# Performance work log

Measured on AMD Instinct MI355X. Metric: run time of the kernel, lower is better.

## Reference

```python
import jax, jax.numpy as jnp
import numpy as np

EPS = 1e-5

def gather_neighbour(pc, idx):
    # pc: [B,N,d], idx: [B,Q,k] -> [B,Q,k,d]
    return jax.vmap(lambda p, i: p[i])(pc, idx)

def rel_pos_encoding(q_xyz, src_xyz, idx):
    # q_xyz: [B,Q,3], src_xyz: [B,N,3], idx: [B,Q,k] -> [B,Q,k,10]
    nbr = gather_neighbour(src_xyz, idx)              # [B,Q,k,3]
    tile = q_xyz[:, :, None, :]                       # [B,Q,1,3]
    rel = tile - nbr                                  # [B,Q,k,3]
    dis = jnp.sqrt(jnp.sum(rel * rel, axis=-1, keepdims=True))
    tile_b = jnp.broadcast_to(tile, nbr.shape)
    return jnp.concatenate([dis, rel, tile_b, nbr], axis=-1)

def conv_bn_relu(x, W, g, b, m, v):
    # 1x1 conv (bias-free) + inference BatchNorm + ReLU; x: [B,Q,K,Cin], W: [Cout,Cin]
    y = jnp.einsum('bqkc,oc->bqko', x, W)
    y = (y - m) * (g * jax.lax.rsqrt(v + EPS)) + b
    return jax.nn.relu(y)

def att_pool(x, Wfc, Wm, g, b, m, v):
    # x: [B,Q,K,C] -> [B,Q,1,Cout]; softmax over neighbor axis K
    att = jnp.einsum('bqkc,oc->bqko', x, Wfc)
    att = jax.nn.softmax(att, axis=2)
    agg = jnp.sum(x * att, axis=2, keepdims=True)     # [B,Q,1,C]
    return conv_bn_relu(agg, Wm, g, b, m, v)

def setup_inputs() -> dict:
    key = jax.random.key(0)
    ks = jax.random.split(key, 40)
    B, Q, k, Nd, Ns = 2, 16384, 16, 4096, 16384
    dim_lb, dim_sc, dim_nl = 128, 64, 128
    d_mid = dim_lb + 10 - dim_sc   # 74
    d_att = dim_lb + 10            # 138
    f32 = jnp.float32
    inp = {}
    inp['features_lb'] = jax.random.normal(ks[0], (B, Q, k, dim_lb), f32)
    inp['features_sc'] = jax.random.normal(ks[1], (B, Q, k, dim_sc), f32)
    inp['NM_lb'] = jax.random.randint(ks[2], (B, Q, k), 0, Nd)
    inp['NM_sc'] = jax.random.randint(ks[3], (B, Q, k), 0, Ns)
    inp['coords_lb'] = jax.random.normal(ks[4], (B, Nd, 3), f32)
    inp['coords_sc'] = jax.random.normal(ks[5], (B, Ns, 3), f32)
    inp['coords_queries'] = jax.random.normal(ks[6], (B, Q, 3), f32)
    inp['NM_cl'] = jax.random.randint(ks[7], (B, Q, k), 0, Q)
    def bn(i, c):
        return (jax.random.uniform(ks[i], (c,), f32) + 0.5,
                jax.random.normal(ks[i + 1], (c,), f32) * 0.1,
                jax.random.normal(ks[i + 2], (c,), f32) * 0.1,
                jax.random.uniform(ks[i + 3], (c,), f32) + 0.5)
    inp['W_lb'] = jax.random.normal(ks[8], (10, 10), f32) * 0.3
    inp['g_lb'], inp['b_lb'], inp['m_lb'], inp['v_lb'] = bn(9, 10)
    inp['W_sc'] = jax.random.normal(ks[13], (d_mid, 10), f32) * 0.3
    inp['g_sc'], inp['b_sc'], inp['m_sc'], inp['v_sc'] = bn(14, d_mid)
    inp['W_fc1'] = jax.random.normal(ks[18], (d_att, d_att), f32) * 0.08
    inp['W_mlp1'] = jax.random.normal(ks[19], (dim_nl, d_att), f32) * 0.08
    inp['g1'], inp['b1'], inp['m1'], inp['v1'] = bn(20, dim_nl)
    inp['W_cl'] = jax.random.normal(ks[24], (10, 10), f32) * 0.3
    inp['g_cl'], inp['b_cl'], inp['m_cl'], inp['v_cl'] = bn(25, 10)
    inp['W_fc2'] = jax.random.normal(ks[29], (d_att, d_att), f32) * 0.08
    inp['W_mlp2'] = jax.random.normal(ks[30], (dim_nl, d_att), f32) * 0.08
    inp['g2'], inp['b2'], inp['m2'], inp['v2'] = bn(31, dim_nl)
    return inp

def reference(features_lb, features_sc, NM_lb, NM_sc, coords_lb, coords_sc,
              coords_queries, NM_cl,
              W_lb, g_lb, b_lb, m_lb, v_lb,
              W_sc, g_sc, b_sc, m_sc, v_sc,
              W_fc1, W_mlp1, g1, b1, m1, v1,
              W_cl, g_cl, b_cl, m_cl, v_cl,
              W_fc2, W_mlp2, g2, b2, m2, v2):
    # branch 1: layer-below
    rppe_lb = conv_bn_relu(rel_pos_encoding(coords_queries, coords_lb, NM_lb),
                           W_lb, g_lb, b_lb, m_lb, v_lb)          # [B,Q,k,10]
    # branch 2: skip connection
    rppe_sc = conv_bn_relu(rel_pos_encoding(coords_queries, coords_sc, NM_sc),
                           W_sc, g_sc, b_sc, m_sc, v_sc)          # [B,Q,k,74]
    locSE_lb = jnp.concatenate([rppe_lb, features_lb], axis=-1)   # [B,Q,k,138]
    locSE_sc = jnp.concatenate([rppe_sc, features_sc], axis=-1)   # [B,Q,k,138]
    f_hat = jnp.concatenate([locSE_lb, locSE_sc], axis=2)         # [B,Q,2k,138]
    f_tilde = att_pool(f_hat, W_fc1, W_mlp1, g1, b1, m1, v1)      # [B,Q,1,128]
    # second aggregation over current layer (num_agg > 1)
    rppe_cl = conv_bn_relu(rel_pos_encoding(coords_queries, coords_queries, NM_cl),
                           W_cl, g_cl, b_cl, m_cl, v_cl)          # [B,Q,k,10]
    f_cur = gather_neighbour(f_tilde[:, :, 0, :], NM_cl)          # [B,Q,k,128]
    locSE_cl = jnp.concatenate([rppe_cl, f_cur], axis=-1)         # [B,Q,k,138]
    f_tilde = att_pool(locSE_cl, W_fc2, W_mlp2, g2, b2, m2, v2)   # [B,Q,1,128]
    # match torch output layout [B, dim_nl, Q, 1]
    return jnp.transpose(f_tilde, (0, 3, 1, 2))
```

## Files before the change

### kernel.cpp

```cpp
#include <hip/hip_runtime.h>
#include <cmath>

#define EPSF 1e-5f
typedef unsigned int  uint32;
typedef unsigned short u16;
typedef __attribute__((ext_vector_type(8))) short bfrag;
typedef __attribute__((ext_vector_type(4))) float f32x4;

constexpr int Qn   = 16384;
constexpr int KS   = 168;
constexpr int PXS  = 42;
constexpr int AGS  = 168;
constexpr int Nd   = 4096;
constexpr float LOG2E = 1.4426950408889634f;

constexpr int OFF_W1  = 0;
constexpr int OFF_WM1 = 23040;
constexpr int OFF_W2  = 43520;
constexpr int OFF_WM2 = 66560;
constexpr int OFF_WLB = 87040;
constexpr int OFF_WSC = 87552;
constexpr int OFF_WCL = 90112;
constexpr int END_W   = 90624;
constexpr int BN_LB = 0;
constexpr int BN_SC = 20;
constexpr int BN_CL = 168;
constexpr int BN_M1 = 188;
constexpr int BN_M2 = 444;
constexpr int BN_TOT = 700;
constexpr int OFF_FT  = END_W + 2 * BN_TOT;
constexpr int PREP_N  = END_W + BN_TOT;

__device__ __forceinline__ u16 f2b(float f) {
    uint32 u = __float_as_uint(f);
    uint32 r = (u + 0x7fffu + ((u >> 16) & 1u)) >> 16;
    return (u16)r;
}
__device__ __forceinline__ float b2f(u16 h) {
    return __uint_as_float(((uint32)h) << 16);
}
__device__ __forceinline__ uint32 cvtpk(float a, float b) {
    uint32 r;
    asm("v_cvt_pk_bf16_f32 %0, %1, %2" : "=v"(r) : "v"(a), "v"(b));
    return r;
}
__device__ __forceinline__ u16 cvt1(float a) { return (u16)cvtpk(a, a); }
__device__ __forceinline__ float exp2_hw(float x) { return __builtin_amdgcn_exp2f(x); }

__global__ __launch_bounds__(256) void prep_weights(
    const float* __restrict__ Wfc1, const float* __restrict__ Wmlp1,
    const float* __restrict__ Wfc2, const float* __restrict__ Wmlp2,
    const float* __restrict__ Wlb,  const float* __restrict__ Wsc,
    const float* __restrict__ Wcl,
    const float* __restrict__ g_lb, const float* __restrict__ b_lb,
    const float* __restrict__ m_lb, const float* __restrict__ v_lb,
    const float* __restrict__ g_sc, const float* __restrict__ b_sc,
    const float* __restrict__ m_sc, const float* __restrict__ v_sc,
    const float* __restrict__ g_cl, const float* __restrict__ b_cl,
    const float* __restrict__ m_cl, const float* __restrict__ v_cl,
    const float* __restrict__ g1, const float* __restrict__ b1,
    const float* __restrict__ m1, const float* __restrict__ v1,
    const float* __restrict__ g2, const float* __restrict__ b2,
    const float* __restrict__ m2, const float* __restrict__ v2,
    u16* __restrict__ ws16)
{
    int i = blockIdx.x * 256 + threadIdx.x;
    if (i >= PREP_N) return;
    if (i >= END_W) {
        int j = i - END_W;
        const float *g, *bb, *m, *v; int o2;
        if (j < BN_SC)      { g = g_lb; bb = b_lb; m = m_lb; v = v_lb; o2 = j - BN_LB; }
        else if (j < BN_CL) { g = g_sc; bb = b_sc; m = m_sc; v = v_sc; o2 = j - BN_SC; }
        else if (j < BN_M1) { g = g_cl; bb = b_cl; m = m_cl; v = v_cl; o2 = j - BN_CL; }
        else if (j < BN_M2) { g = g1;   bb = b1;   m = m1;   v = v1;   o2 = j - BN_M1; }
        else                { g = g2;   bb = b2;   m = m2;   v = v2;   o2 = j - BN_M2; }
        int o = o2 >> 1;
        float sc_ = g[o] * rsqrtf(v[o] + EPSF);
        ((float*)(ws16 + END_W))[j] = (o2 & 1) ? (bb[o] - m[o] * sc_) : sc_;
        return;
    }
    int lane = (i >> 3) & 63, jj = i & 7;
    int row16 = lane & 15;
    int kf = ((lane >> 4) << 3) + jj;
    float v = 0.f;
    if (i < OFF_WLB) {
        const float* src; int nrows; int idx; bool fc = false;
        if (i < OFF_WM1)      { src = Wfc1;  nrows = 138; idx = i - OFF_W1;  fc = true; }
        else if (i < OFF_W2)  { src = Wmlp1; nrows = 128; idx = i - OFF_WM1; }
        else if (i < OFF_WM2) { src = Wfc2;  nrows = 138; idx = i - OFF_W2;  fc = true; }
        else                  { src = Wmlp2; nrows = 128; idx = i - OFF_WM2; }
        int t = idx >> 9, nt = t / 5, kt = t - nt * 5;
        int row = nt * 16 + row16;
        int kp  = kt * 32 + kf;
        int k   = (kp < 10) ? kp : kp - 2;
        if (row < nrows && kp < 140 && kp != 10 && kp != 11) {
            v = src[row * 138 + k];
            if (fc) v *= LOG2E;
        }
    } else {
        const float* src; int nrows; int idx;
        if (i < OFF_WSC)      { src = Wlb; nrows = 10; idx = i - OFF_WLB; }
        else if (i < OFF_WCL) { src = Wsc; nrows = 74; idx = i - OFF_WSC; }
        else                  { src = Wcl; nrows = 10; idx = i - OFF_WCL; }
        int t = idx >> 9;
        int row = t * 16 + row16;
        if (row < nrows && kf < 10) v = src[row * 10 + kf];
    }
    ws16[i] = f2b(v);
}

__device__ __forceinline__ void loadB(bfrag (&bf)[5], const u16* __restrict__ Wt,
                                      int nt, int lane) {
    #pragma unroll
    for (int kt = 0; kt < 5; ++kt)
        bf[kt] = *(const bfrag*)&Wt[((nt * 5 + kt) << 9) + (lane << 3)];
}
__device__ __forceinline__ void mfma32(const bfrag (&af)[2][5], const bfrag (&bf)[5],
                                       f32x4 &a0, f32x4 &a1) {
    const f32x4 zf = {0.f, 0.f, 0.f, 0.f};
    a0 = zf; a1 = zf;
    #pragma unroll
    for (int kt = 0; kt < 5; ++kt) {
        a0 = __builtin_amdgcn_mfma_f32_16x16x32_bf16(af[0][kt], bf[kt], a0, 0, 0, 0);
        a1 = __builtin_amdgcn_mfma_f32_16x16x32_bf16(af[1][kt], bf[kt], a1, 0, 0, 0);
    }
}
__device__ __forceinline__ void mfma16(const bfrag (&af)[5], const bfrag (&bf)[5],
                                       f32x4 &a0) {
    const f32x4 zf = {0.f, 0.f, 0.f, 0.f};
    a0 = zf;
    #pragma unroll
    for (int kt = 0; kt < 5; ++kt)
        a0 = __builtin_amdgcn_mfma_f32_16x16x32_bf16(af[kt], bf[kt], a0, 0, 0, 0);
}
__device__ __forceinline__ void soft32(
    const f32x4& a0, const f32x4& a1, int nt,
    int lane, int lrow, const u16* __restrict__ fr0, const u16* __restrict__ fr1,
    u16* __restrict__ ag)
{
    const int ch  = nt * 16 + lrow;
    const int chp = ch + (ch >= 10 ? 2 : 0);
    float s = 0.f, num = 0.f;
    #pragma unroll
    for (int r = 0; r < 4; ++r) {
        float e = exp2_hw(a0[r]);
        s += e;
        num += e * b2f(fr0[r * KS + chp]);
    }
    #pragma unroll
    for (int r = 0; r < 4; ++r) {
        float e = exp2_hw(a1[r]);
        s += e;
        num += e * b2f(fr1[r * KS + chp]);
    }
    s   += __shfl_xor(s, 16);   s   += __shfl_xor(s, 32);
    num += __shfl_xor(num, 16); num += __shfl_xor(num, 32);
    if (lane < 16)
        ag[chp] = cvt1((ch < 138) ? num * __builtin_amdgcn_rcpf(s) : 0.f);
}
__device__ __forceinline__ void soft16(
    const f32x4& a0, int nt,
    int lane, int lrow, const u16* __restrict__ fr0, u16* __restrict__ ag)
{
    const int ch  = nt * 16 + lrow;
    const int chp = ch + (ch >= 10 ? 2 : 0);
    float s = 0.f, num = 0.f;
    #pragma unroll
    for (int r = 0; r < 4; ++r) {
        float e = exp2_hw(a0[r]);
        s += e;
        num += e * b2f(fr0[r * KS + chp]);
    }
    s   += __shfl_xor(s, 16);   s   += __shfl_xor(s, 32);
    num += __shfl_xor(num, 16); num += __shfl_xor(num, 32);
    if (lane < 16)
        ag[chp] = cvt1((ch < 138) ? num * __builtin_amdgcn_rcpf(s) : 0.f);
}
#define SB() __builtin_amdgcn_sched_barrier(0)

__global__ __launch_bounds__(256, 4) void stage1(
    const float* __restrict__ feat_lb, const float* __restrict__ feat_sc,
    const int* __restrict__ nm_lb, const int* __restrict__ nm_sc,
    const float* __restrict__ c_lb, const float* __restrict__ c_sc,
    const float* __restrict__ c_q,
    u16* __restrict__ ws16)
{
    __shared__ __align__(16) u16 fhat[64 * KS];
    __shared__ __align__(16) u16 pxs[64 * PXS];
    u16* aggs = pxs;

    const int tid  = threadIdx.x;
    const int bq0  = blockIdx.x * 2;
    const int b    = bq0 >> 14;
    const int lane = tid & 63;
    const int w    = tid >> 6;
    const int lrow = lane & 15;
    const int lgr  = lane >> 4;
    const int q    = w >> 1;
    const int h    = w & 1;

    const u16* W1t  = ws16 + OFF_W1;
    const u16* Wm1t = ws16 + OFF_WM1;
    const float* bn = (const float*)(ws16 + END_W);
    u16* ft = ws16 + OFF_FT;

    bfrag wcv[3];
    float2 bnv[3];
    if (h == 0) {
        wcv[0] = *(const bfrag*)&ws16[OFF_WLB + (lane << 3)];
        wcv[1] = *(const bfrag*)&ws16[OFF_WSC + (lane << 3)];
        wcv[2] = *(const bfrag*)&ws16[OFF_WSC + 512 + (lane << 3)];
        bnv[0] = (lrow < 10) ? *(const float2*)&bn[BN_LB + lrow * 2] : float2{0.f, 0.f};
        bnv[1] = *(const float2*)&bn[BN_SC + lrow * 2];
        bnv[2] = *(const float2*)&bn[BN_SC + (16 + lrow) * 2];
    } else {
        #pragma unroll
        for (int t = 0; t < 3; ++t) {
            wcv[t] = *(const bfrag*)&ws16[OFF_WSC + ((2 + t) << 9) + (lane << 3)];
            int o = (2 + t) * 16 + lrow;
            bnv[t] = (o < 74) ? *(const float2*)&bn[BN_SC + o * 2] : float2{0.f, 0.f};
        }
    }

    {
        const float4* flb = (const float4*)(feat_lb + (size_t)bq0 * 2048);
        float4 r0[4];
        #pragma unroll
        for (int it = 0; it < 4; ++it) r0[it] = flb[tid + it * 256];
        const float4* fsc = (const float4*)(feat_sc + (size_t)bq0 * 1024);
        float4 r1[2];
        #pragma unroll
        for (int it = 0; it < 2; ++it) r1[it] = fsc[tid + it * 256];
        #pragma unroll
        for (int it = 0; it < 4; ++it) {
            int u = tid + it * 256;
            int qq = u >> 9, rem = u & 511, r = rem >> 5, c4 = rem & 31;
            uint32* d = (uint32*)&fhat[(qq * 32 + r) * KS + 12 + c4 * 4];
            d[0] = cvtpk(r0[it].x, r0[it].y); d[1] = cvtpk(r0[it].z, r0[it].w);
        }
        #pragma unroll
        for (int it = 0; it < 2; ++it) {
            int u = tid + it * 256;
            int qq = u >> 8, rem = u & 255, r = rem >> 4, c4 = rem & 15;
            uint32* d = (uint32*)&fhat[(qq * 32 + 16 + r) * KS + 76 + c4 * 4];
            d[0] = cvtpk(r1[it].x, r1[it].y); d[1] = cvtpk(r1[it].z, r1[it].w);
        }
        for (int u = tid; u < 64 * 15; u += 256) {
            int row = u / 15, jj = u - row * 15;
            uint32* base = (uint32*)((char*)fhat + row * 336);
            if (jj == 0) base[5] = 0u; else base[69 + jj] = 0u;
        }
    }
    if (tid < 64) {
        const int qq = tid >> 5, r = tid & 31;
        const int bq = bq0 + qq;
        const bool lb = r < 16;
        const int idx = lb ? nm_lb[bq * 16 + r] : nm_sc[bq * 16 + (r - 16)];
        const float* nb = lb ? (c_lb + ((size_t)b * Nd + idx) * 3)
                             : (c_sc + ((size_t)b * Qn + idx) * 3);
        const float qx = c_q[bq * 3 + 0], qy = c_q[bq * 3 + 1], qz = c_q[bq * 3 + 2];
        const float nx = nb[0], ny = nb[1], nz = nb[2];
        const float rx = qx - nx, ry = qy - ny, rz = qz - nz;
        const float dd = sqrtf(rx * rx + ry * ry + rz * rz);
        uint32* pw = (uint32*)&pxs[tid * PXS];
        pw[0] = cvtpk(dd, rx); pw[1] = cvtpk(ry, rz); pw[2] = cvtpk(qx, qy);
        pw[3] = cvtpk(qz, nx); pw[4] = cvtpk(ny, nz);
        #pragma unroll
        for (int z = 5; z < 16; ++z) pw[z] = 0u;
    }
    __syncthreads();

    const f32x4 zf = {0.f, 0.f, 0.f, 0.f};

    {
        bfrag pa1 = *(const bfrag*)&pxs[(q * 32 + 16 + lrow) * PXS + lgr * 8];
        if (h == 0) {
            bfrag pa0 = *(const bfrag*)&pxs[(q * 32 + lrow) * PXS + lgr * 8];
            f32x4 c = __builtin_amdgcn_mfma_f32_16x16x32_bf16(pa0, wcv[0], zf, 0, 0, 0);
            if (lrow < 10) {
                #pragma unroll
                for (int r = 0; r < 4; ++r)
                    fhat[(q * 32 + lgr * 4 + r) * KS + lrow] =
                        cvt1(fmaxf(c[r] * bnv[0].x + bnv[0].y, 0.f));
            }
            #pragma unroll
            for (int t = 1; t < 3; ++t) {
                f32x4 c2 = __builtin_amdgcn_mfma_f32_16x16x32_bf16(pa1, wcv[t], zf, 0, 0, 0);
                const int o  = (t - 1) * 16 + lrow;
                const int cp = (o < 10) ? o : o + 2;
                #pragma unroll
                for (int r = 0; r < 4; ++r)
                    fhat[(q * 32 + 16 + lgr * 4 + r) * KS + cp] =
                        cvt1(fmaxf(c2[r] * bnv[t].x + bnv[t].y, 0.f));
            }
        } else {
            #pragma unroll
            for (int t = 0; t < 3; ++t) {
                f32x4 c2 = __builtin_amdgcn_mfma_f32_16x16x32_bf16(pa1, wcv[t], zf, 0, 0, 0);
                const int o = (2 + t) * 16 + lrow;
                if (o < 74) {
                    #pragma unroll
                    for (int r = 0; r < 4; ++r)
                        fhat[(q * 32 + 16 + lgr * 4 + r) * KS + o + 2] =
                            cvt1(fmaxf(c2[r] * bnv[t].x + bnv[t].y, 0.f));
                }
            }
        }
    }
    __syncthreads();

    bfrag af[2][5];
    #pragma unroll
    for (int mt = 0; mt < 2; ++mt)
        #pragma unroll
        for (int kt = 0; kt < 5; ++kt)
            af[mt][kt] = *(const bfrag*)&fhat[(q * 32 + mt * 16 + lrow) * KS + kt * 32 + lgr * 8];

    const u16* fr0 = fhat + (q * 32 + lgr * 4) * KS;
    const u16* fr1 = fr0 + 16 * KS;
    u16* ag = aggs + q * AGS;

    bfrag b0[5], b1[5];
    f32x4 a0, a1;
    if (h == 0) {
        loadB(b0, W1t, 0, lane);
        loadB(b1, W1t, 1, lane); mfma32(af, b0, a0, a1); SB(); soft32(a0, a1, 0, lane, lrow, fr0, fr1, ag);
        loadB(b0, W1t, 2, lane); mfma32(af, b1, a0, a1); SB(); soft32(a0, a1, 1, lane, lrow, fr0, fr1, ag);
        loadB(b1, W1t, 3, lane); mfma32(af, b0, a0, a1); SB(); soft32(a0, a1, 2, lane, lrow, fr0, fr1, ag);
        loadB(b0, W1t, 4, lane); mfma32(af, b1, a0, a1); SB(); soft32(a0, a1, 3, lane, lrow, fr0, fr1, ag);
        mfma32(af, b0, a0, a1); soft32(a0, a1, 4, lane, lrow, fr0, fr1, ag);
        if (lane < 2)       ag[10 + lane] = 0;
        else if (lane < 16) ag[144 + lane] = 0;
    } else {
        loadB(b0, W1t, 5, lane);
        loadB(b1, W1t, 6, lane); mfma32(af, b0, a0, a1); SB(); soft32(a0, a1, 5, lane, lrow, fr0, fr1, ag);
        loadB(b0, W1t, 7, lane); mfma32(af, b1, a0, a1); SB(); soft32(a0, a1, 6, lane, lrow, fr0, fr1, ag);
        loadB(b1, W1t, 8, lane); mfma32(af, b0, a0, a1); SB(); soft32(a0, a1, 7, lane, lrow, fr0, fr1, ag);
        mfma32(af, b1, a0, a1); soft32(a0, a1, 8, lane, lrow, fr0, fr1, ag);
    }
    __syncthreads();

    bfrag am[5];
    #pragma unroll
    for (int kt = 0; kt < 5; ++kt)
        am[kt] = *(const bfrag*)&aggs[lrow * AGS + kt * 32 + lgr * 8];
    #pragma unroll
    for (int oi = 0; oi < 2; ++oi) {
        const int ot = w * 2 + oi;
        f32x4 c = zf;
        #pragma unroll
        for (int kt = 0; kt < 5; ++kt) {
            bfrag wm = *(const bfrag*)&Wm1t[(((ot * 5) + kt) << 9) + (lane << 3)];
            c = __builtin_amdgcn_mfma_f32_16x16x32_bf16(am[kt], wm, c, 0, 0, 0);
        }
        if (lgr == 0) {
            const int o = ot * 16 + lrow;
            float2 p = *(const float2*)&bn[BN_M1 + o * 2];
            #pragma unroll
            for (int r = 0; r < 2; ++r)
                ft[(size_t)(bq0 + r) * 128 + o] = cvt1(fmaxf(c[r] * p.x + p.y, 0.f));
        }
    }
}

__global__ __launch_bounds__(512, 4) void stage2(
    const int* __restrict__ nm_cl, const float* __restrict__ c_q,
    const u16* __restrict__ ws16, float* __restrict__ out)
{
    __shared__ __align__(16) u16 fhat[128 * KS];
    __shared__ __align__(16) u16 pxs[128 * PXS];
    u16* aggs = pxs;

    const int tid  = threadIdx.x;
    const int bq0  = blockIdx.x * 8;
    const int b    = bq0 >> 14;
    const int q0   = bq0 & (Qn - 1);
    const int lane = tid & 63;
    const int w    = tid >> 6;
    const int lrow = lane & 15;
    const int lgr  = lane >> 4;

    const u16* W2t  = ws16 + OFF_W2;
    const u16* Wm2t = ws16 + OFF_WM2;
    const float* bn = (const float*)(ws16 + END_W);
    const u16* ft   = ws16 + OFF_FT;

    bfrag wcl = *(const bfrag*)&ws16[OFF_WCL + (lane << 3)];
    float2 bncl = (lrow < 10) ? *(const float2*)&bn[BN_CL + lrow * 2] : float2{0.f, 0.f};

    for (int u = tid; u < 128 * 15; u += 512) {
        int row = u / 15, jj = u - row * 15;
        uint32* base = (uint32*)((char*)fhat + row * 336);
        if (jj == 0) base[5] = 0u; else base[69 + jj] = 0u;
    }
    if (tid < 128) {
        const int qq = tid >> 4, r = tid & 15;
        const int bq = bq0 + qq;
        const int idx = nm_cl[bq * 16 + r];
        const float* nb = c_q + ((size_t)(b << 14) + idx) * 3;
        const float qx = c_q[bq * 3 + 0], qy = c_q[bq * 3 + 1], qz = c_q[bq * 3 + 2];
        const float nx = nb[0], ny = nb[1], nz = nb[2];
        const float rx = qx - nx, ry = qy - ny, rz = qz - nz;
        const float dd = sqrtf(rx * rx + ry * ry + rz * rz);
        uint32* pw = (uint32*)&pxs[tid * PXS];
        pw[0] = cvtpk(dd, rx); pw[1] = cvtpk(ry, rz); pw[2] = cvtpk(qx, qy);
        pw[3] = cvtpk(qz, nx); pw[4] = cvtpk(ny, nz);
        #pragma unroll
        for (int z = 5; z < 16; ++z) pw[z] = 0u;
    }
    #pragma unroll
    for (int i = 0; i < 16; ++i) {
        int u = tid + i * 512;
        int row = u >> 6, c2 = u & 63;
        int qq = row >> 4;
        int idx = nm_cl[(bq0 + qq) * 16 + (row & 15)];
        const uint32* srow = (const uint32*)(ft + (size_t)((b << 14) + idx) * 128);
        *(uint32*)&fhat[row * KS + 12 + c2 * 2] = srow[c2];
    }
    __syncthreads();

    const f32x4 zf = {0.f, 0.f, 0.f, 0.f};

    {
        bfrag pa = *(const bfrag*)&pxs[(w * 16 + lrow) * PXS + lgr * 8];
        f32x4 c = __builtin_amdgcn_mfma_f32_16x16x32_bf16(pa, wcl, zf, 0, 0, 0);
        if (lrow < 10) {
            #pragma unroll
            for (int r = 0; r < 4; ++r)
                fhat[(w * 16 + lgr * 4 + r) * KS + lrow] =
                    cvt1(fmaxf(c[r] * bncl.x + bncl.y, 0.f));
        }
    }
    __syncthreads();

    bfrag af[5];
    #pragma unroll
    for (int kt = 0; kt < 5; ++kt)
        af[kt] = *(const bfrag*)&fhat[(w * 16 + lrow) * KS + kt * 32 + lgr * 8];

    const u16* fr0 = fhat + (w * 16 + lgr * 4) * KS;
    u16* ag = aggs + w * AGS;

    bfrag b0[5], b1[5];
    f32x4 a0;
    loadB(b0, W2t, 0, lane);
    loadB(b1, W2t, 1, lane); mfma16(af, b0, a0); SB(); soft16(a0, 0, lane, lrow, fr0, ag);
    loadB(b0, W2t, 2, lane); mfma16(af, b1, a0); SB(); soft16(a0, 1, lane, lrow, fr0, ag);
    loadB(b1, W2t, 3, lane); mfma16(af, b0, a0); SB(); soft16(a0, 2, lane, lrow, fr0, ag);
    loadB(b0, W2t, 4, lane); mfma16(af, b1, a0); SB(); soft16(a0, 3, lane, lrow, fr0, ag);
    loadB(b1, W2t, 5, lane); mfma16(af, b0, a0); SB(); soft16(a0, 4, lane, lrow, fr0, ag);
    loadB(b0, W2t, 6, lane); mfma16(af, b1, a0); SB(); soft16(a0, 5, lane, lrow, fr0, ag);
    loadB(b1, W2t, 7, lane); mfma16(af, b0, a0); SB(); soft16(a0, 6, lane, lrow, fr0, ag);
    loadB(b0, W2t, 8, lane); mfma16(af, b1, a0); SB(); soft16(a0, 7, lane, lrow, fr0, ag);
    mfma16(af, b0, a0); soft16(a0, 8, lane, lrow, fr0, ag);
    if (lane < 2)       ag[10 + lane] = 0;
    else if (lane < 16) ag[144 + lane] = 0;
    __syncthreads();

    bfrag am[5];
    #pragma unroll
    for (int kt = 0; kt < 5; ++kt)
        am[kt] = *(const bfrag*)&aggs[lrow * AGS + kt * 32 + lgr * 8];
    {
        f32x4 c = zf;
        #pragma unroll
        for (int kt = 0; kt < 5; ++kt) {
            bfrag wm = *(const bfrag*)&Wm2t[(((w * 5) + kt) << 9) + (lane << 3)];
            c = __builtin_amdgcn_mfma_f32_16x16x32_bf16(am[kt], wm, c, 0, 0, 0);
        }
        if (lgr < 2) {
            const int o = w * 16 + lrow;
            float2 p = *(const float2*)&bn[BN_M2 + o * 2];
            #pragma unroll
            for (int r = 0; r < 4; ++r) {
                const int qloc = lgr * 4 + r;
                out[((size_t)(b * 128 + o) << 14) + q0 + qloc] = fmaxf(c[r] * p.x + p.y, 0.f);
            }
        }
    }
}

extern "C" void kernel_launch(void* const* d_in, const int* in_sizes, int n_in,
                              void* d_out, int out_size, void* d_ws, size_t ws_size,
                              hipStream_t stream)
{
    const float* feat_lb = (const float*)d_in[0];
    const float* feat_sc = (const float*)d_in[1];
    const int*   nm_lb   = (const int*)d_in[2];
    const int*   nm_sc   = (const int*)d_in[3];
    const float* c_lb    = (const float*)d_in[4];
    const float* c_sc    = (const float*)d_in[5];
    const float* c_q     = (const float*)d_in[6];
    const int*   nm_cl   = (const int*)d_in[7];
    const float* W_lb = (const float*)d_in[8];
    const float* g_lb = (const float*)d_in[9];
    const float* b_lb = (const float*)d_in[10];
    const float* m_lb = (const float*)d_in[11];
    const float* v_lb = (const float*)d_in[12];
    const float* W_sc = (const float*)d_in[13];
    const float* g_sc = (const float*)d_in[14];
    const float* b_sc = (const float*)d_in[15];
    const float* m_sc = (const float*)d_in[16];
    const float* v_sc = (const float*)d_in[17];
    const float* W_fc1  = (const float*)d_in[18];
    const float* W_mlp1 = (const float*)d_in[19];
    const float* g1 = (const float*)d_in[20];
    const float* b1 = (const float*)d_in[21];
    const float* m1 = (const float*)d_in[22];
    const float* v1 = (const float*)d_in[23];
    const float* W_cl = (const float*)d_in[24];
    const float* g_cl = (const float*)d_in[25];
    const float* b_cl = (const float*)d_in[26];
    const float* m_cl = (const float*)d_in[27];
    const float* v_cl = (const float*)d_in[28];
    const float* W_fc2  = (const float*)d_in[29];
    const float* W_mlp2 = (const float*)d_in[30];
    const float* g2 = (const float*)d_in[31];
    const float* b2 = (const float*)d_in[32];
    const float* m2 = (const float*)d_in[33];
    const float* v2 = (const float*)d_in[34];

    u16* ws16 = (u16*)d_ws;
    float* out = (float*)d_out;

    hipLaunchKernelGGL(prep_weights, dim3((PREP_N + 255) / 256), dim3(256), 0, stream,
        W_fc1, W_mlp1, W_fc2, W_mlp2, W_lb, W_sc, W_cl,
        g_lb, b_lb, m_lb, v_lb, g_sc, b_sc, m_sc, v_sc,
        g_cl, b_cl, m_cl, v_cl, g1, b1, m1, v1, g2, b2, m2, v2, ws16);

    hipLaunchKernelGGL(stage1, dim3(2 * Qn / 2), dim3(256), 0, stream,
        feat_lb, feat_sc, nm_lb, nm_sc, c_lb, c_sc, c_q, ws16);

    hipLaunchKernelGGL(stage2, dim3(2 * Qn / 8), dim3(512), 0, stream,
        nm_cl, c_q, ws16, out);
}
```

Measured before the change: 225.3 us.

## Switch stage1 attention to 32x32 MFMA, one query per block, split out MLP kernel

Stage1 now processes one query per 128-thread block, not two per 256-thread block. The attention logits are computed with 32x32x16 bf16 MFMAs over the 32 neighbours, using a new repacked fc1 weight layout built by an extra prep kernel. The aggregated features are written to a global workspace, and the following MLP+BN+ReLU runs in a separate mlp1 kernel that batches 16 queries per wave. This fills whole MFMA tiles in the MLP and cuts shuffle reductions in the softmax, at the cost of an extra global round trip for the aggregates and two more kernel launches.

Result: no change. 229.4 us (+1.8%).

```diff
diff --git a/kernel.cpp b/kernel.cpp
--- a/kernel.cpp
+++ b/kernel.cpp
@@ -6,6 +6,7 @@
 typedef unsigned short u16;
 typedef __attribute__((ext_vector_type(8))) short bfrag;
 typedef __attribute__((ext_vector_type(4))) float f32x4;
+typedef __attribute__((ext_vector_type(16))) float f32x16;
 
 constexpr int Qn   = 16384;
 constexpr int KS   = 168;
@@ -29,6 +30,9 @@
 constexpr int BN_M2 = 444;
 constexpr int BN_TOT = 700;
 constexpr int OFF_FT  = END_W + 2 * BN_TOT;
+constexpr int OFF_AG  = OFF_FT + 2 * Qn * 128;
+constexpr int OFF_W32 = OFF_AG + 2 * Qn * AGS;
+constexpr int N_W32   = 2 * 5 * 10 * 512;
 constexpr int PREP_N  = END_W + BN_TOT;
 
 __device__ __forceinline__ u16 f2b(float f) {
@@ -109,21 +113,30 @@
     ws16[i] = f2b(v);
 }
 
+__global__ __launch_bounds__(256) void prep_weights32(
+    const float* __restrict__ Wfc1, const float* __restrict__ Wfc2,
+    u16* __restrict__ ws16)
+{
+    int i = blockIdx.x * 256 + threadIdx.x;
+    if (i >= N_W32) return;
+    const float* src = (i < N_W32 / 2) ? Wfc1 : Wfc2;
+    int idx = (i < N_W32 / 2) ? i : i - N_W32 / 2;
+    int t = idx >> 9;
+    int lane = (idx >> 3) & 63, j = idx & 7;
+    int nt = t / 10, kt = t - nt * 10;
+    int o  = nt * 32 + (lane & 31);
+    int kp = kt * 16 + ((lane >> 5) << 3) + j;
+    int k  = (kp < 10) ? kp : kp - 2;
+    float v = 0.f;
+    if (o < 138 && kp < 140 && kp != 10 && kp != 11) v = src[o * 138 + k] * LOG2E;
+    ws16[OFF_W32 + i] = f2b(v);
+}
+
 __device__ __forceinline__ void loadB(bfrag (&bf)[5], const u16* __restrict__ Wt,
                                       int nt, int lane) {
     #pragma unroll
     for (int kt = 0; kt < 5; ++kt)
         bf[kt] = *(const bfrag*)&Wt[((nt * 5 + kt) << 9) + (lane << 3)];
-}
-__device__ __forceinline__ void mfma32(const bfrag (&af)[2][5], const bfrag (&bf)[5],
-                                       f32x4 &a0, f32x4 &a1) {
-    const f32x4 zf = {0.f, 0.f, 0.f, 0.f};
-    a0 = zf; a1 = zf;
-    #pragma unroll
-    for (int kt = 0; kt < 5; ++kt) {
-        a0 = __builtin_amdgcn_mfma_f32_16x16x32_bf16(af[0][kt], bf[kt], a0, 0, 0, 0);
-        a1 = __builtin_amdgcn_mfma_f32_16x16x32_bf16(af[1][kt], bf[kt], a1, 0, 0, 0);
-    }
 }
 __device__ __forceinline__ void mfma16(const bfrag (&af)[5], const bfrag (&bf)[5],
                                        f32x4 &a0) {
@@ -133,10 +146,9 @@
     for (int kt = 0; kt < 5; ++kt)
         a0 = __builtin_amdgcn_mfma_f32_16x16x32_bf16(af[kt], bf[kt], a0, 0, 0, 0);
 }
-__device__ __forceinline__ void soft32(
-    const f32x4& a0, const f32x4& a1, int nt,
-    int lane, int lrow, const u16* __restrict__ fr0, const u16* __restrict__ fr1,
-    u16* __restrict__ ag)
+__device__ __forceinline__ void soft16(
+    const f32x4& a0, int nt,
+    int lane, int lrow, const u16* __restrict__ fr0, u16* __restrict__ ag)
 {
     const int ch  = nt * 16 + lrow;
     const int chp = ch + (ch >= 10 ? 2 : 0);
@@ -147,62 +159,62 @@
         s += e;
         num += e * b2f(fr0[r * KS + chp]);
     }
-    #pragma unroll
-    for (int r = 0; r < 4; ++r) {
-        float e = exp2_hw(a1[r]);
-        s += e;
-        num += e * b2f(fr1[r * KS + chp]);
-    }
     s   += __shfl_xor(s, 16);   s   += __shfl_xor(s, 32);
     num += __shfl_xor(num, 16); num += __shfl_xor(num, 32);
     if (lane < 16)
         ag[chp] = cvt1((ch < 138) ? num * __builtin_amdgcn_rcpf(s) : 0.f);
 }
-__device__ __forceinline__ void soft16(
-    const f32x4& a0, int nt,
-    int lane, int lrow, const u16* __restrict__ fr0, u16* __restrict__ ag)
-{
-    const int ch  = nt * 16 + lrow;
+#define SB() __builtin_amdgcn_sched_barrier(0)
+
+__device__ __forceinline__ void unit32(
+    int nt, const bfrag (&af32)[10], const u16* __restrict__ W32,
+    int lane, const u16* __restrict__ frh, u16* __restrict__ ag)
+{
+    f32x16 acc;
+    #pragma unroll
+    for (int r = 0; r < 16; ++r) acc[r] = 0.f;
+    #pragma unroll
+    for (int kt = 0; kt < 10; ++kt) {
+        bfrag bf = *(const bfrag*)&W32[((nt * 10 + kt) << 9) + (lane << 3)];
+        acc = __builtin_amdgcn_mfma_f32_32x32x16_bf16(af32[kt], bf, acc, 0, 0, 0);
+    }
+    const int ch  = nt * 32 + (lane & 31);
     const int chp = ch + (ch >= 10 ? 2 : 0);
     float s = 0.f, num = 0.f;
     #pragma unroll
-    for (int r = 0; r < 4; ++r) {
-        float e = exp2_hw(a0[r]);
+    for (int reg = 0; reg < 16; ++reg) {
+        float e = exp2_hw(acc[reg]);
         s += e;
-        num += e * b2f(fr0[r * KS + chp]);
-    }
-    s   += __shfl_xor(s, 16);   s   += __shfl_xor(s, 32);
-    num += __shfl_xor(num, 16); num += __shfl_xor(num, 32);
-    if (lane < 16)
+        const int brow = (reg & 3) + 8 * (reg >> 2);
+        num += e * b2f(frh[brow * KS + chp]);
+    }
+    s   += __shfl_xor(s, 32);
+    num += __shfl_xor(num, 32);
+    if (lane < 32)
         ag[chp] = cvt1((ch < 138) ? num * __builtin_amdgcn_rcpf(s) : 0.f);
 }
-#define SB() __builtin_amdgcn_sched_barrier(0)
-
-__global__ __launch_bounds__(256, 4) void stage1(
+
+__global__ __launch_bounds__(128, 8) void stage1(
     const float* __restrict__ feat_lb, const float* __restrict__ feat_sc,
     const int* __restrict__ nm_lb, const int* __restrict__ nm_sc,
     const float* __restrict__ c_lb, const float* __restrict__ c_sc,
     const float* __restrict__ c_q,
     u16* __restrict__ ws16)
 {
-    __shared__ __align__(16) u16 fhat[64 * KS];
-    __shared__ __align__(16) u16 pxs[64 * PXS];
-    u16* aggs = pxs;
+    __shared__ __align__(16) u16 fhat[32 * KS];
+    __shared__ __align__(16) u16 pxs[32 * PXS];
 
     const int tid  = threadIdx.x;
-    const int bq0  = blockIdx.x * 2;
-    const int b    = bq0 >> 14;
+    const int bq   = blockIdx.x;
+    const int b    = bq >> 14;
     const int lane = tid & 63;
-    const int w    = tid >> 6;
+    const int h    = tid >> 6;
     const int lrow = lane & 15;
     const int lgr  = lane >> 4;
-    const int q    = w >> 1;
-    const int h    = w & 1;
-
-    const u16* W1t  = ws16 + OFF_W1;
-    const u16* Wm1t = ws16 + OFF_WM1;
+
+    const u16* W32  = ws16 + OFF_W32;
     const float* bn = (const float*)(ws16 + END_W);
-    u16* ft = ws16 + OFF_FT;
+    u16* ag = ws16 + OFF_AG + (size_t)bq * AGS;
 
     bfrag wcv[3];
     float2 bnv[3];
@@ -223,37 +235,40 @@
     }
 
     {
-        const float4* flb = (const float4*)(feat_lb + (size_t)bq0 * 2048);
+        const float4* flb = (const float4*)(feat_lb + (size_t)bq * 2048);
         float4 r0[4];
         #pragma unroll
-        for (int it = 0; it < 4; ++it) r0[it] = flb[tid + it * 256];
-        const float4* fsc = (const float4*)(feat_sc + (size_t)bq0 * 1024);
+        for (int it = 0; it < 4; ++it) r0[it] = flb[tid + it * 128];
+        const float4* fsc = (const float4*)(feat_sc + (size_t)bq * 1024);
         float4 r1[2];
         #pragma unroll
-        for (int it = 0; it < 2; ++it) r1[it] = fsc[tid + it * 256];
+        for (int it = 0; it < 2; ++it) r1[it] = fsc[tid + it * 128];
         #pragma unroll
         for (int it = 0; it < 4; ++it) {
-            int u = tid + it * 256;
-            int qq = u >> 9, rem = u & 511, r = rem >> 5, c4 = rem & 31;
-            uint32* d = (uint32*)&fhat[(qq * 32 + r) * KS + 12 + c4 * 4];
+            int u = tid + it * 128;
+            int nbr = u >> 5, c4 = u & 31;
+            uint32* d = (uint32*)&fhat[nbr * KS + 12 + c4 * 4];
             d[0] = cvtpk(r0[it].x, r0[it].y); d[1] = cvtpk(r0[it].z, r0[it].w);
         }
         #pragma unroll
         for (int it = 0; it < 2; ++it) {
-            int u = tid + it * 256;
-            int qq = u >> 8, rem = u & 255, r = rem >> 4, c4 = rem & 15;
-            uint32* d = (uint32*)&fhat[(qq * 32 + 16 + r) * KS + 76 + c4 * 4];
+            int u = tid + it * 128;
+            int nbr = u >> 4, c4 = u & 15;
+            uint32* d = (uint32*)&fhat[(16 + nbr) * KS + 76 + c4 * 4];
             d[0] = cvtpk(r1[it].x, r1[it].y); d[1] = cvtpk(r1[it].z, r1[it].w);
         }
-        for (int u = tid; u < 64 * 15; u += 256) {
-            int row = u / 15, jj = u - row * 15;
-            uint32* base = (uint32*)((char*)fhat + row * 336);
-            if (jj == 0) base[5] = 0u; else base[69 + jj] = 0u;
-        }
-    }
-    if (tid < 64) {
-        const int qq = tid >> 5, r = tid & 31;
-        const int bq = bq0 + qq;
+        if (tid < 32) ((uint32*)((char*)fhat + tid * 336))[5] = 0u;
+        #pragma unroll
+        for (int it = 0; it < 4; ++it) {
+            int u = tid + it * 128;
+            if (u < 448) {
+                int row = u / 14, jj = u - row * 14;
+                ((uint32*)((char*)fhat + row * 336))[70 + jj] = 0u;
+            }
+        }
+    }
+    if (tid < 32) {
+        const int r = tid;
         const bool lb = r < 16;
         const int idx = lb ? nm_lb[bq * 16 + r] : nm_sc[bq * 16 + (r - 16)];
         const float* nb = lb ? (c_lb + ((size_t)b * Nd + idx) * 3)
@@ -273,14 +288,14 @@
     const f32x4 zf = {0.f, 0.f, 0.f, 0.f};
 
     {
-        bfrag pa1 = *(const bfrag*)&pxs[(q * 32 + 16 + lrow) * PXS + lgr * 8];
+        bfrag pa1 = *(const bfrag*)&pxs[(16 + lrow) * PXS + lgr * 8];
         if (h == 0) {
-            bfrag pa0 = *(const bfrag*)&pxs[(q * 32 + lrow) * PXS + lgr * 8];
+            bfrag pa0 = *(const bfrag*)&pxs[lrow * PXS + lgr * 8];
             f32x4 c = __builtin_amdgcn_mfma_f32_16x16x32_bf16(pa0, wcv[0], zf, 0, 0, 0);
             if (lrow < 10) {
                 #pragma unroll
                 for (int r = 0; r < 4; ++r)
-                    fhat[(q * 32 + lgr * 4 + r) * KS + lrow] =
+                    fhat[(lgr * 4 + r) * KS + lrow] =
                         cvt1(fmaxf(c[r] * bnv[0].x + bnv[0].y, 0.f));
             }
             #pragma unroll
@@ -290,7 +305,7 @@
                 const int cp = (o < 10) ? o : o + 2;
                 #pragma unroll
                 for (int r = 0; r < 4; ++r)
-                    fhat[(q * 32 + 16 + lgr * 4 + r) * KS + cp] =
+                    fhat[(16 + lgr * 4 + r) * KS + cp] =
                         cvt1(fmaxf(c2[r] * bnv[t].x + bnv[t].y, 0.f));
             }
         } else {
@@ -301,7 +316,7 @@
                 if (o < 74) {
                     #pragma unroll
                     for (int r = 0; r < 4; ++r)
-                        fhat[(q * 32 + 16 + lgr * 4 + r) * KS + o + 2] =
+                        fhat[(16 + lgr * 4 + r) * KS + o + 2] =
                             cvt1(fmaxf(c2[r] * bnv[t].x + bnv[t].y, 0.f));
                 }
             }
@@ -309,56 +324,58 @@
     }
     __syncthreads();
 
-    bfrag af[2][5];
-    #pragma unroll
-    for (int mt = 0; mt < 2; ++mt)
+    bfrag af32[10];
+    #pragma unroll
+    for (int kt = 0; kt < 10; ++kt)
+        af32[kt] = *(const bfrag*)&fhat[(lane & 31) * KS + kt * 16 + ((lane >> 5) << 3)];
+    const u16* frh = fhat + (lane >> 5) * 4 * KS;
+
+    if (h == 0) {
+        unit32(0, af32, W32, lane, frh, ag);
+        unit32(1, af32, W32, lane, frh, ag);
+        unit32(2, af32, W32, lane, frh, ag);
+        if (lane < 2) ag[10 + lane] = 0;
+    } else {
+        unit32(3, af32, W32, lane, frh, ag);
+        unit32(4, af32, W32, lane, frh, ag);
+    }
+}
+
+__global__ __launch_bounds__(256) void mlp1(const u16* __restrict__ ws16,
+                                            u16* __restrict__ ws16w)
+{
+    const int tid  = threadIdx.x;
+    const int lane = tid & 63;
+    const int w    = tid >> 6;
+    const int lrow = lane & 15;
+    const int lgr  = lane >> 4;
+    const int q0   = (blockIdx.x * 4 + w) * 16;
+
+    const u16* Wm = ws16 + OFF_WM1;
+    const float* bn = (const float*)(ws16 + END_W);
+    const u16* agg = ws16 + OFF_AG;
+    u16* ftg = ws16w + OFF_FT;
+
+    bfrag af[5];
+    #pragma unroll
+    for (int kt = 0; kt < 5; ++kt)
+        af[kt] = *(const bfrag*)&agg[(size_t)(q0 + lrow) * AGS + kt * 32 + lgr * 8];
+
+    const f32x4 zf = {0.f, 0.f, 0.f, 0.f};
+    #pragma unroll
+    for (int ot = 0; ot < 8; ++ot) {
+        bfrag bf[5];
+        loadB(bf, Wm, ot, lane);
+        f32x4 c = zf;
         #pragma unroll
         for (int kt = 0; kt < 5; ++kt)
-            af[mt][kt] = *(const bfrag*)&fhat[(q * 32 + mt * 16 + lrow) * KS + kt * 32 + lgr * 8];
-
-    const u16* fr0 = fhat + (q * 32 + lgr * 4) * KS;
-    const u16* fr1 = fr0 + 16 * KS;
-    u16* ag = aggs + q * AGS;
-
-    bfrag b0[5], b1[5];
-    f32x4 a0, a1;
-    if (h == 0) {
-        loadB(b0, W1t, 0, lane);
-        loadB(b1, W1t, 1, lane); mfma32(af, b0, a0, a1); SB(); soft32(a0, a1, 0, lane, lrow, fr0, fr1, ag);
-        loadB(b0, W1t, 2, lane); mfma32(af, b1, a0, a1); SB(); soft32(a0, a1, 1, lane, lrow, fr0, fr1, ag);
-        loadB(b1, W1t, 3, lane); mfma32(af, b0, a0, a1); SB(); soft32(a0, a1, 2, lane, lrow, fr0, fr1, ag);
-        loadB(b0, W1t, 4, lane); mfma32(af, b1, a0, a1); SB(); soft32(a0, a1, 3, lane, lrow, fr0, fr1, ag);
-        mfma32(af, b0, a0, a1); soft32(a0, a1, 4, lane, lrow, fr0, fr1, ag);
-        if (lane < 2)       ag[10 + lane] = 0;
-        else if (lane < 16) ag[144 + lane] = 0;
-    } else {
-        loadB(b0, W1t, 5, lane);
-        loadB(b1, W1t, 6, lane); mfma32(af, b0, a0, a1); SB(); soft32(a0, a1, 5, lane, lrow, fr0, fr1, ag);
-        loadB(b0, W1t, 7, lane); mfma32(af, b1, a0, a1); SB(); soft32(a0, a1, 6, lane, lrow, fr0, fr1, ag);
-        loadB(b1, W1t, 8, lane); mfma32(af, b0, a0, a1); SB(); soft32(a0, a1, 7, lane, lrow, fr0, fr1, ag);
-        mfma32(af, b1, a0, a1); soft32(a0, a1, 8, lane, lrow, fr0, fr1, ag);
-    }
-    __syncthreads();
-
-    bfrag am[5];
-    #pragma unroll
-    for (int kt = 0; kt < 5; ++kt)
-        am[kt] = *(const bfrag*)&aggs[lrow * AGS + kt * 32 + lgr * 8];
-    #pragma unroll
-    for (int oi = 0; oi < 2; ++oi) {
-        const int ot = w * 2 + oi;
-        f32x4 c = zf;
-        #pragma unroll
-        for (int kt = 0; kt < 5; ++kt) {
-            bfrag wm = *(const bfrag*)&Wm1t[(((ot * 5) + kt) << 9) + (lane << 3)];
-            c = __builtin_amdgcn_mfma_f32_16x16x32_bf16(am[kt], wm, c, 0, 0, 0);
-        }
-        if (lgr == 0) {
-            const int o = ot * 16 + lrow;
-            float2 p = *(const float2*)&bn[BN_M1 + o * 2];
-            #pragma unroll
-            for (int r = 0; r < 2; ++r)
-                ft[(size_t)(bq0 + r) * 128 + o] = cvt1(fmaxf(c[r] * p.x + p.y, 0.f));
+            c = __builtin_amdgcn_mfma_f32_16x16x32_bf16(af[kt], bf[kt], c, 0, 0, 0);
+        const int o = ot * 16 + lrow;
+        float2 p = *(const float2*)&bn[BN_M1 + o * 2];
+        #pragma unroll
+        for (int r = 0; r < 4; ++r) {
+            int q = q0 + lgr * 4 + r;
+            ftg[(size_t)q * 128 + o] = cvt1(fmaxf(c[r] * p.x + p.y, 0.f));
         }
     }
 }
@@ -528,8 +545,13 @@
         g_lb, b_lb, m_lb, v_lb, g_sc, b_sc, m_sc, v_sc,
         g_cl, b_cl, m_cl, v_cl, g1, b1, m1, v1, g2, b2, m2, v2, ws16);
 
-    hipLaunchKernelGGL(stage1, dim3(2 * Qn / 2), dim3(256), 0, stream,
+    hipLaunchKernelGGL(prep_weights32, dim3((N_W32 + 255) / 256), dim3(256), 0, stream,
+        W_fc1, W_fc2, ws16);
+
+    hipLaunchKernelGGL(stage1, dim3(2 * Qn), dim3(128), 0, stream,
         feat_lb, feat_sc, nm_lb, nm_sc, c_lb, c_sc, c_q, ws16);
+
+    hipLaunchKernelGGL(mlp1, dim3(2 * Qn / 64), dim3(256), 0, stream, ws16, ws16);
 
     hipLaunchKernelGGL(stage2, dim3(2 * Qn / 8), dim3(512), 0, stream,
         nm_cl, c_q, ws16, out);
```
